# Kernel tuning notes

Measured on AMD Instinct MI355X. Metric: run time of the kernel, lower is better.

Reference implementation:

```python
import jax, jax.numpy as jnp
import numpy as np
import math

B, T, N, D = 8, 4, 2048, 256
M, E = 4096, 8

def setup_inputs() -> dict:
    key = jax.random.key(0)
    ks = jax.random.split(key, 8)
    std = 0.02
    return {
        "prop_embed": jax.random.normal(ks[0], (B, T, N, D), jnp.float32),
        "adap_embed": jax.random.normal(ks[1], (B, N, D), jnp.float32),
        "x_proj_w": jax.random.normal(ks[2], (D, D), jnp.float32) * (1.0 / np.sqrt(D)),
        "x_proj_b": jnp.zeros((D,), jnp.float32),
        "keyMatrix": jax.random.normal(ks[3], (M, D), jnp.float32) * std,
        "memMatrix": jax.random.normal(ks[4], (M, D), jnp.float32) * std,
        "w_gate": jax.random.normal(ks[5], (D, E), jnp.float32) * (1.0 / np.sqrt(D)),
        "w_noise": jax.random.normal(ks[6], (D, E), jnp.float32) * (1.0 / np.sqrt(D)),
    }

def reference(prop_embed, adap_embed, x_proj_w, x_proj_b, keyMatrix, memMatrix, w_gate, w_noise):
    b, t, n, d = prop_embed.shape
    m = memMatrix.shape[0]
    x = jnp.mean(prop_embed, axis=1)                      # [B,N,D]
    q = jnp.tanh(x @ x_proj_w.T + x_proj_b)               # [B,N,D]
    att = jnp.einsum('bnd,md->bnm', q, keyMatrix)         # [B,N,M]
    # eval mode: noise_stddev * self.training == 0, so noisy_logits == clean_logits
    clean_logits = memMatrix @ w_gate                     # [M,E]
    mem_label = jax.nn.softmax(clean_logits, axis=-1)     # [M,E]
    # sparse_qk: keep top-k = int(ln(M)) logits, rest -> -inf
    k = int(math.log(m))
    vals, idx = jax.lax.top_k(att, k)                     # [B,N,k]
    att2 = jnp.full((b * n, m), -jnp.inf, dtype=att.dtype)
    rows = jnp.arange(b * n)[:, None]
    att2 = att2.at[rows, idx.reshape(b * n, k)].set(vals.reshape(b * n, k))
    att_w = jax.nn.softmax(att2, axis=-1).reshape(b, n, m)
    mem_retrieved = jnp.einsum('bnm,md->bnd', att_w, memMatrix)
    label_retrieved = jnp.einsum('bnm,me->bne', att_w, mem_label)
    gate = label_retrieved
    return (gate, mem_retrieved, label_retrieved, mem_label, att_w)
```

## Files before the change

### kernel.cpp

```cpp
#include <hip/hip_runtime.h>
#include <hip/hip_fp16.h>
#include <math.h>

#define Bb 8
#define Tt 4
#define Nn 2048
#define Dd 256
#define Mm 4096
#define Ee 8
#define ROWS (Bb*Nn)
#define KSEL 8
#define KC 16

#define O_GATE 0LL
#define O_MEMR 131072LL
#define O_LABR 4325376LL
#define O_MLAB 4456448LL
#define O_ATTW 4489216LL

#define WS_WT    0LL
#define WS_KH    262144LL
#define WS_ATTH  16777216LL
#define WS_QH    150994944LL

typedef float f32x4 __attribute__((ext_vector_type(4)));
typedef short short8 __attribute__((ext_vector_type(8)));
typedef _Float16 f16x8 __attribute__((ext_vector_type(8)));

__device__ __forceinline__ unsigned short f2h(float x) {
    __half h = __float2half(x);
    return *reinterpret_cast<unsigned short*>(&h);
}

__device__ __forceinline__ void gload_lds16(const void* g, void* l) {
    __builtin_amdgcn_global_load_lds(
        (const __attribute__((address_space(1))) unsigned int*)g,
        (__attribute__((address_space(3))) unsigned int*)l,
        16, 0, 0);
}

__global__ __launch_bounds__(256) void k_prep(const float* __restrict__ W, float* __restrict__ WT,
                                              const float* __restrict__ key, unsigned short* __restrict__ kh,
                                              const float* __restrict__ mem, const float* __restrict__ wg,
                                              float* __restrict__ mlab) {
    int b = blockIdx.x, tid = threadIdx.x;
    if (b < 256) {
        int i = b * 256 + tid;
        int r = i >> 8, c = i & 255;
        WT[c * 256 + r] = W[r * 256 + c];
    } else if (b < 256 + 4096) {
        int idx = (b - 256) * 256 + tid;
        kh[idx] = f2h(key[idx]);
    } else {
        int m = (b - 4352) * 256 + tid;
        if (m < Mm) {
            float acc[Ee];
            #pragma unroll
            for (int e = 0; e < Ee; ++e) acc[e] = 0.f;
            const float* mr = mem + (long long)m * Dd;
            for (int d = 0; d < Dd; ++d) {
                float mv = mr[d];
                #pragma unroll
                for (int e = 0; e < Ee; ++e) acc[e] = fmaf(mv, wg[d * Ee + e], acc[e]);
            }
            float mx = acc[0];
            #pragma unroll
            for (int e = 1; e < Ee; ++e) mx = fmaxf(mx, acc[e]);
            float z = 0.f;
            #pragma unroll
            for (int e = 0; e < Ee; ++e) { acc[e] = expf(acc[e] - mx); z += acc[e]; }
            float inv = 1.f / z;
            #pragma unroll
            for (int e = 0; e < Ee; ++e) mlab[(long long)m * Ee + e] = acc[e] * inv;
        }
    }
}

__global__ __launch_bounds__(256) void k_q(const float* __restrict__ prop,
                                           const float* __restrict__ WT,
                                           const float* __restrict__ bias,
                                           float* __restrict__ qf,
                                           unsigned short* __restrict__ qh) {
    __shared__ float xs[16][256];
    int tid = threadIdx.x;
    int row0 = blockIdx.x * 16;
    #pragma unroll
    for (int r = 0; r < 16; ++r) {
        int row = row0 + r;
        int b = row >> 11;
        int n = row & 2047;
        const float* p = prop + ((long long)(b * Tt) * Nn + n) * Dd + tid;
        float s = 0.f;
        #pragma unroll
        for (int t = 0; t < Tt; ++t) s += p[(long long)t * Nn * Dd];
        xs[r][tid] = s * 0.25f;
    }
    __syncthreads();
    float acc[16];
    #pragma unroll
    for (int r = 0; r < 16; ++r) acc[r] = 0.f;
    int c = tid;
    for (int d = 0; d < 256; ++d) {
        float wv = WT[d * 256 + c];
        #pragma unroll
        for (int r = 0; r < 16; ++r) acc[r] = fmaf(xs[r][d], wv, acc[r]);
    }
    float bv = bias[c];
    #pragma unroll
    for (int r = 0; r < 16; ++r) {
        float qv = tanhf(acc[r] + bv);
        long long o = (long long)(row0 + r) * Dd + c;
        qf[o] = qv;
        qh[o] = f2h(qv);
    }
}

__global__ __launch_bounds__(256) void k_att(const unsigned short* __restrict__ qh,
                                             const unsigned short* __restrict__ kh,
                                             unsigned short* __restrict__ attH) {
    __shared__ __align__(16) unsigned short smem[17408];
    int bid = blockIdx.x;
    int swz = (bid & 7) * 512 + (bid >> 3);
    int bx = swz & 31;
    int by = swz >> 5;
    int tid = threadIdx.x;
    int lane = tid & 63, w = tid >> 6;
    int wr = w >> 1, wc = w & 1;
    long long row0 = (long long)by * 128;
    long long col0 = (long long)bx * 128;

    f32x4 acc[4][4];
    #pragma unroll
    for (int m = 0; m < 4; ++m)
        #pragma unroll
        for (int n = 0; n < 4; ++n) acc[m][n] = (f32x4){0.f, 0.f, 0.f, 0.f};

    int rr = lane >> 2;
    int sp = lane & 3;

    auto stage = [&](int k0) {
        #pragma unroll
        for (int t = 0; t < 2; ++t) {
            const unsigned short* src = t ? kh : qh;
            long long b0 = t ? col0 : row0;
            #pragma unroll
            for (int i = 0; i < 2; ++i) {
                int r = w * 32 + i * 16 + rr;
                int sl = sp ^ ((r >> 1) & 3);
                const unsigned short* g = src + (b0 + r) * 256 + k0 * 32 + sl * 8;
                unsigned short* l = smem + t * 4096 + (w * 32 + i * 16) * 32;
                gload_lds16(g, l);
            }
        }
    };

    stage(0);
    for (int k0 = 0; k0 < 8; ++k0) {
        __syncthreads();
        int lr = lane & 15, j = lane >> 4;
        f16x8 ah[4], bh[4];
        #pragma unroll
        for (int m = 0; m < 4; ++m) {
            int r = wr * 64 + m * 16 + lr;
            int off = r * 32 + ((j ^ ((r >> 1) & 3)) * 8);
            ah[m] = *(const f16x8*)(smem + off);
        }
        #pragma unroll
        for (int n = 0; n < 4; ++n) {
            int r = wc * 64 + n * 16 + lr;
            int off = r * 32 + ((j ^ ((r >> 1) & 3)) * 8);
            bh[n] = *(const f16x8*)(smem + 4096 + off);
        }
        #pragma unroll
        for (int m = 0; m < 4; ++m)
            #pragma unroll
            for (int n = 0; n < 4; ++n)
                acc[m][n] = __builtin_amdgcn_mfma_f32_16x16x32_f16(ah[m], bh[n], acc[m][n], 0, 0, 0);
        if (k0 < 7) { __syncthreads(); stage(k0 + 1); }
    }

    __syncthreads();
    {
        int lr = lane & 15, j = lane >> 4;
        #pragma unroll
        for (int m = 0; m < 4; ++m)
            #pragma unroll
            for (int n = 0; n < 4; ++n) {
                int c = wc * 64 + n * 16 + lr;
                #pragma unroll
                for (int reg = 0; reg < 4; ++reg) {
                    int r = wr * 64 + m * 16 + j * 4 + reg;
                    smem[r * 136 + c] = f2h(acc[m][n][reg]);
                }
            }
    }
    __syncthreads();
    {
        int tr = tid >> 4;
        int tc = tid & 15;
        #pragma unroll
        for (int pass = 0; pass < 8; ++pass) {
            int r = pass * 16 + tr;
            short8 vv = *(const short8*)(smem + r * 136 + tc * 8);
            *(short8*)(attH + (row0 + r) * Mm + col0 + tc * 8) = vv;
        }
    }
}

__global__ __launch_bounds__(256) void k_final2(const unsigned short* __restrict__ attH,
                                                const float* __restrict__ qf,
                                                const float* __restrict__ key,
                                                const float* __restrict__ mem,
                                                const float* __restrict__ mlab,
                                                float* __restrict__ gate,
                                                float* __restrict__ memr,
                                                float* __restrict__ labr,
                                                float* __restrict__ attw) {
    int tid = threadIdx.x;
    int lane = tid & 63;
    long long row = (long long)blockIdx.x * 4 + (tid >> 6);
    const unsigned short* arow = attH + row * Mm;

    unsigned int v[8];
    #pragma unroll
    for (int s = 0; s < 8; ++s) v[s] = 0u;

    #pragma unroll
    for (int t = 0; t < 8; ++t) {
        int c8 = t * 64 + lane;
        short8 x8 = *(const short8*)(arow + c8 * 8);
        unsigned int rb = (unsigned)(4095 - c8 * 8);
        #pragma unroll
        for (int jj = 0; jj < 8; ++jj) {
            unsigned int b = (unsigned short)x8[jj];
            unsigned int sr = (unsigned)((int)(b << 16) >> 31);
            unsigned int mono = b ^ ((sr >> 17) | 0x8000u);
            unsigned int keyv = (mono << 16) | (rb - jj);
            if (keyv > v[7]) {
                unsigned int x = keyv;
                #pragma unroll
                for (int s = 0; s < 8; ++s) {
                    unsigned int hi = v[s] > x ? v[s] : x;
                    unsigned int lo = v[s] > x ? x : v[s];
                    v[s] = hi; x = lo;
                }
            }
        }
    }

    unsigned int sk[KC];
    #pragma unroll
    for (int k = 0; k < KC; ++k) {
        unsigned int bv = v[0];
        #pragma unroll
        for (int d = 1; d < 64; d <<= 1) {
            unsigned int ov = (unsigned)__shfl_xor((int)bv, d);
            bv = bv > ov ? bv : ov;
        }
        sk[k] = bv;
        bool won = (v[0] == bv);
        #pragma unroll
        for (int s = 0; s < 7; ++s) v[s] = won ? v[s + 1] : v[s];
        v[7] = won ? 0u : v[7];
    }

    int civ[KC];
    #pragma unroll
    for (int s = 0; s < KC; ++s) civ[s] = 4095 - (int)(sk[s] & 0xFFFFu);

    int c = lane & 15, g = lane >> 4;
    int cidx = civ[0];
    #pragma unroll
    for (int s = 1; s < KC; ++s) cidx = (c == s) ? civ[s] : cidx;
    const float* qrow = qf + row * Dd;
    const float* krow = key + (long long)cidx * Dd;
    double dacc = 0.0;
    #pragma unroll
    for (int i = 0; i < 16; ++i) {
        float4 qv = *(const float4*)(qrow + g * 64 + i * 4);
        float4 kv = *(const float4*)(krow + g * 64 + i * 4);
        dacc = fma((double)qv.x, (double)kv.x, dacc);
        dacc = fma((double)qv.y, (double)kv.y, dacc);
        dacc = fma((double)qv.z, (double)kv.z, dacc);
        dacc = fma((double)qv.w, (double)kv.w, dacc);
    }
    dacc += __shfl_xor(dacc, 16);
    dacc += __shfl_xor(dacc, 32);
    float rvf = (float)dacc;

    float cv[KC];
    #pragma unroll
    for (int s = 0; s < KC; ++s) cv[s] = __shfl(rvf, s);

    unsigned int m32[KC];
    #pragma unroll
    for (int s = 0; s < KC; ++s) {
        unsigned int fb = __float_as_uint(cv[s]);
        m32[s] = fb ^ ((unsigned)((int)fb >> 31) | 0x80000000u);
    }
    bool sel[KC];
    #pragma unroll
    for (int s = 0; s < KC; ++s) {
        int r = 0;
        #pragma unroll
        for (int t = 0; t < KC; ++t) {
            if (t != s) {
                bool gt = (m32[t] > m32[s]) || (m32[t] == m32[s] && civ[t] < civ[s]);
                r += gt ? 1 : 0;
            }
        }
        sel[s] = (r < KSEL);
    }

    float mx = cv[0];
    #pragma unroll
    for (int s = 1; s < KC; ++s) mx = fmaxf(mx, cv[s]);
    float p[KC]; float z = 0.f;
    #pragma unroll
    for (int s = 0; s < KC; ++s) { p[s] = sel[s] ? expf(cv[s] - mx) : 0.f; z += p[s]; }
    float inv = 1.f / z;
    #pragma unroll
    for (int s = 0; s < KC; ++s) p[s] *= inv;

    {
        float4 a = make_float4(0.f, 0.f, 0.f, 0.f);
        #pragma unroll
        for (int s = 0; s < KC; ++s) {
            if (sel[s]) {
                const float4 mv = *(const float4*)(mem + (long long)civ[s] * Dd + lane * 4);
                a.x = fmaf(p[s], mv.x, a.x); a.y = fmaf(p[s], mv.y, a.y);
                a.z = fmaf(p[s], mv.z, a.z); a.w = fmaf(p[s], mv.w, a.w);
            }
        }
        *(float4*)(memr + row * Dd + lane * 4) = a;
    }

    if (lane < Ee) {
        float s8 = 0.f;
        #pragma unroll
        for (int s = 0; s < KC; ++s)
            if (sel[s]) s8 = fmaf(p[s], mlab[(long long)civ[s] * Ee + lane], s8);
        gate[row * Ee + lane] = s8;
        labr[row * Ee + lane] = s8;
    }

    float* awrow = attw + row * Mm;
    {
        f32x4 zz = (f32x4){0.f, 0.f, 0.f, 0.f};
        #pragma unroll
        for (int t = 0; t < 16; ++t)
            __builtin_nontemporal_store(zz, (f32x4*)(awrow + (t * 64 + lane) * 4));
    }
    __syncthreads();
    if (lane < KC) {
        float myp = p[0]; int myi = civ[0];
        #pragma unroll
        for (int s = 1; s < KC; ++s) {
            myp = (lane == s) ? p[s] : myp;
            myi = (lane == s) ? civ[s] : myi;
        }
        awrow[myi] = myp;
    }
}

extern "C" void kernel_launch(void* const* d_in, const int* in_sizes, int n_in,
                              void* d_out, int out_size, void* d_ws, size_t ws_size,
                              hipStream_t stream) {
    const float* prop = (const float*)d_in[0];
    const float* W    = (const float*)d_in[2];
    const float* bias = (const float*)d_in[3];
    const float* key  = (const float*)d_in[4];
    const float* mem  = (const float*)d_in[5];
    const float* wg   = (const float*)d_in[6];

    float* out  = (float*)d_out;
    float* gate = out + O_GATE;
    float* memr = out + O_MEMR;
    float* labr = out + O_LABR;
    float* mlab = out + O_MLAB;
    float* attw = out + O_ATTW;

    char* ws = (char*)d_ws;
    float*          WT   = (float*)(ws + WS_WT);
    unsigned short* kh   = (unsigned short*)(ws + WS_KH);
    unsigned short* attH = (unsigned short*)(ws + WS_ATTH);
    unsigned short* qh   = (unsigned short*)(ws + WS_QH);
    float*          qf   = memr;

    k_prep<<<4368, 256, 0, stream>>>(W, WT, key, kh, mem, wg, mlab);
    k_q<<<ROWS / 16, 256, 0, stream>>>(prop, WT, bias, qf, qh);
    k_att<<<4096, 256, 0, stream>>>(qh, kh, attH);
    k_final2<<<ROWS / 4, 256, 0, stream>>>(attH, qf, key, mem, mlab, gate, memr, labr, attw);
}
```

Measured before the change: 274.1 us.

## Fuse per-tile top-8 candidate selection into attention GEMM epilogue

The attention GEMM kernel no longer writes the full fp16 score matrix to global memory. Each block now selects the top-8 candidates per row within its 128-column tile from a bank-swizzled LDS copy. It writes only those packed keys, and the final kernel merges 32 tile candidate lists per row. This removes a 128MB write and read of intermediate scores at the cost of extra selection work in the GEMM epilogue. The key index field in the merge step is now masked to 12 bits.

```diff
diff --git a/kernel.cpp b/kernel.cpp
--- a/kernel.cpp
+++ b/kernel.cpp
@@ -20,7 +20,7 @@
 
 #define WS_WT    0LL
 #define WS_KH    262144LL
-#define WS_ATTH  16777216LL
+#define WS_CAND  16777216LL
 #define WS_QH    150994944LL
 
 typedef float f32x4 __attribute__((ext_vector_type(4)));
@@ -117,7 +117,7 @@
 
 __global__ __launch_bounds__(256) void k_att(const unsigned short* __restrict__ qh,
                                              const unsigned short* __restrict__ kh,
-                                             unsigned short* __restrict__ attH) {
+                                             unsigned int* __restrict__ cand) {
     __shared__ __align__(16) unsigned short smem[17408];
     int bid = blockIdx.x;
     int swz = (bid & 7) * 512 + (bid >> 3);
@@ -190,24 +190,59 @@
                 #pragma unroll
                 for (int reg = 0; reg < 4; ++reg) {
                     int r = wr * 64 + m * 16 + j * 4 + reg;
-                    smem[r * 136 + c] = f2h(acc[m][n][reg]);
+                    int pc = (((c >> 3) ^ (r & 7)) << 3) | (c & 7);
+                    smem[r * 136 + pc] = f2h(acc[m][n][reg]);
                 }
             }
     }
     __syncthreads();
+
     {
-        int tr = tid >> 4;
-        int tc = tid & 15;
-        #pragma unroll
-        for (int pass = 0; pass < 8; ++pass) {
-            int r = pass * 16 + tr;
-            short8 vv = *(const short8*)(smem + r * 136 + tc * 8);
-            *(short8*)(attH + (row0 + r) * Mm + col0 + tc * 8) = vv;
-        }
-    }
-}
-
-__global__ __launch_bounds__(256) void k_final2(const unsigned short* __restrict__ attH,
+        int r2 = tid >> 1;
+        int hf = tid & 1;
+        unsigned int v[8];
+        #pragma unroll
+        for (int s = 0; s < 8; ++s) v[s] = 0u;
+
+        #pragma unroll
+        for (int t8 = 0; t8 < 8; ++t8) {
+            int slot = hf * 8 + t8;
+            short8 x8 = *(const short8*)(smem + r2 * 136 + ((slot ^ (r2 & 7)) << 3));
+            int gc0 = (int)col0 + slot * 8;
+            #pragma unroll
+            for (int jj = 0; jj < 8; ++jj) {
+                unsigned int b = (unsigned short)x8[jj];
+                unsigned int sr = (unsigned)((int)(b << 16) >> 31);
+                unsigned int mono = b ^ ((sr >> 17) | 0x8000u);
+                unsigned int keyv = (mono << 16) | (unsigned)(4095 - (gc0 + jj));
+                if (keyv > v[7]) {
+                    unsigned int x = keyv;
+                    #pragma unroll
+                    for (int s = 0; s < 8; ++s) {
+                        unsigned int hi = v[s] > x ? v[s] : x;
+                        unsigned int lo = v[s] > x ? x : v[s];
+                        v[s] = hi; x = lo;
+                    }
+                }
+            }
+        }
+        unsigned int nv[8];
+        #pragma unroll
+        for (int s = 0; s < 8; ++s) {
+            unsigned int pv = (unsigned)__shfl_xor((int)v[7 - s], 1);
+            nv[s] = v[s] > pv ? v[s] : pv;
+        }
+        if (hf == 0) {
+            unsigned int* dst = cand + ((long long)bx * ROWS + row0 + r2) * 8;
+            uint4 a = make_uint4(nv[0], nv[1], nv[2], nv[3]);
+            uint4 bq = make_uint4(nv[4], nv[5], nv[6], nv[7]);
+            *(uint4*)dst = a;
+            *(uint4*)(dst + 4) = bq;
+        }
+    }
+}
+
+__global__ __launch_bounds__(256) void k_final2(const unsigned int* __restrict__ cand,
                                                 const float* __restrict__ qf,
                                                 const float* __restrict__ key,
                                                 const float* __restrict__ mem,
@@ -219,31 +254,23 @@
     int tid = threadIdx.x;
     int lane = tid & 63;
     long long row = (long long)blockIdx.x * 4 + (tid >> 6);
-    const unsigned short* arow = attH + row * Mm;
-
-    unsigned int v[8];
-    #pragma unroll
-    for (int s = 0; s < 8; ++s) v[s] = 0u;
-
-    #pragma unroll
-    for (int t = 0; t < 8; ++t) {
-        int c8 = t * 64 + lane;
-        short8 x8 = *(const short8*)(arow + c8 * 8);
-        unsigned int rb = (unsigned)(4095 - c8 * 8);
-        #pragma unroll
-        for (int jj = 0; jj < 8; ++jj) {
-            unsigned int b = (unsigned short)x8[jj];
-            unsigned int sr = (unsigned)((int)(b << 16) >> 31);
-            unsigned int mono = b ^ ((sr >> 17) | 0x8000u);
-            unsigned int keyv = (mono << 16) | (rb - jj);
-            if (keyv > v[7]) {
-                unsigned int x = keyv;
-                #pragma unroll
-                for (int s = 0; s < 8; ++s) {
-                    unsigned int hi = v[s] > x ? v[s] : x;
-                    unsigned int lo = v[s] > x ? x : v[s];
-                    v[s] = hi; x = lo;
-                }
+
+    int tl = lane >> 1, of = (lane & 1) * 4;
+    uint4 kk = *(const uint4*)(cand + ((long long)tl * ROWS + row) * 8 + of);
+
+    unsigned int v[4];
+    #pragma unroll
+    for (int s = 0; s < 4; ++s) v[s] = 0u;
+    {
+        unsigned int ins[4] = {kk.x, kk.y, kk.z, kk.w};
+        #pragma unroll
+        for (int i = 0; i < 4; ++i) {
+            unsigned int x = ins[i];
+            #pragma unroll
+            for (int s = 0; s < 4; ++s) {
+                unsigned int hi = v[s] > x ? v[s] : x;
+                unsigned int lo = v[s] > x ? x : v[s];
+                v[s] = hi; x = lo;
             }
         }
     }
@@ -259,14 +286,15 @@
         }
         sk[k] = bv;
         bool won = (v[0] == bv);
-        #pragma unroll
-        for (int s = 0; s < 7; ++s) v[s] = won ? v[s + 1] : v[s];
-        v[7] = won ? 0u : v[7];
+        v[0] = won ? v[1] : v[0];
+        v[1] = won ? v[2] : v[1];
+        v[2] = won ? v[3] : v[2];
+        v[3] = won ? 0u : v[3];
     }
 
     int civ[KC];
     #pragma unroll
-    for (int s = 0; s < KC; ++s) civ[s] = 4095 - (int)(sk[s] & 0xFFFFu);
+    for (int s = 0; s < KC; ++s) civ[s] = 4095 - (int)(sk[s] & 0xFFFu);
 
     int c = lane & 15, g = lane >> 4;
     int cidx = civ[0];
@@ -383,12 +411,12 @@
     char* ws = (char*)d_ws;
     float*          WT   = (float*)(ws + WS_WT);
     unsigned short* kh   = (unsigned short*)(ws + WS_KH);
-    unsigned short* attH = (unsigned short*)(ws + WS_ATTH);
+    unsigned int*   cand = (unsigned int*)(ws + WS_CAND);
     unsigned short* qh   = (unsigned short*)(ws + WS_QH);
     float*          qf   = memr;
 
     k_prep<<<4368, 256, 0, stream>>>(W, WT, key, kh, mem, wg, mlab);
     k_q<<<ROWS / 16, 256, 0, stream>>>(prop, WT, bias, qf, qh);
-    k_att<<<4096, 256, 0, stream>>>(qh, kh, attH);
-    k_final2<<<ROWS / 4, 256, 0, stream>>>(attH, qf, key, mem, mlab, gate, memr, labr, attw);
-}
+    k_att<<<4096, 256, 0, stream>>>(qh, kh, cand);
+    k_final2<<<ROWS / 4, 256, 0, stream>>>(cand, qf, key, mem, mlab, gate, memr, labr, attw);
+}
```

After: 263.6 us. 3.8% less time.
